# Performance work log

Hardware: AMD Instinct MI355X
Metric: run time of the kernel (lower is better)

The kernel has to match this reference:

```python
import jax, jax.numpy as jnp
import numpy as np

N_LAYERS = 2
N_COEF = 5
IN_DIM = 256
LN_EPS = 1e-6  # flax LayerNorm default


def jacobi_design(x, a, n):
    """Jacobi polynomials P_0..P_{n-1}^{(a,a)}(x). x: [...], returns [..., n]."""
    Ps = [jnp.ones_like(x)]
    if n > 1:
        Ps.append((a + 1.0) * x)
    for k in range(2, n):
        t = 2.0 * k + 2.0 * a
        A = 2.0 * k * (k + 2.0 * a) * (t - 2.0)
        B = (t - 1.0) * t * (t - 2.0)
        C = 2.0 * (k + a - 1.0) ** 2 * t
        Ps.append((B * x * Ps[-1] - C * Ps[-2]) / A)
    return jnp.stack(Ps, axis=-1)


def setup_inputs() -> dict:
    key = jax.random.key(0)
    k1, k2 = jax.random.split(key)
    x = jax.random.normal(k1, (8192, IN_DIM), dtype=jnp.float32)
    coefs = jax.random.normal(k2, (N_LAYERS, IN_DIM, IN_DIM, N_COEF), dtype=jnp.float32) * 0.03
    alphas = jnp.zeros((N_LAYERS,), dtype=jnp.float32)      # alpha_arctanh init zeros
    ln_scale = jnp.ones((N_LAYERS, IN_DIM), dtype=jnp.float32)
    ln_bias = jnp.zeros((N_LAYERS, IN_DIM), dtype=jnp.float32)
    return {"x": x, "coefs": coefs, "alphas": alphas, "ln_scale": ln_scale, "ln_bias": ln_bias}


def reference(x, coefs, alphas, ln_scale, ln_bias):
    h = x  # [B, D]
    for l in range(N_LAYERS):
        # LayerNorm
        mu = jnp.mean(h, axis=-1, keepdims=True)
        var = jnp.mean(jnp.square(h - mu), axis=-1, keepdims=True)
        hn = (h - mu) * jax.lax.rsqrt(var + LN_EPS) * ln_scale[l] + ln_bias[l]
        # KANLayer: Jacobi design matrix on tanh-mapped input
        a = jnp.tanh(alphas[l])
        dm = jacobi_design(jnp.tanh(hn), a, N_COEF)  # [B, D, C]
        # resid_scale=0, spline_scale=1, dropout inactive -> y = mean_i einsum
        in_dim = hn.shape[-1]
        h = jnp.einsum('bic,ioc->bo', dm, coefs[l]) / in_dim  # [B, D]
    return h
```

## Files before the change

kernel.cpp:

```cpp
#include <hip/hip_runtime.h>

#define D 256
#define NB 8192
#define NKC 128
#define PANEL (NKC * 512)

#define SXX_STRIDE 264
#define SXX_ELEMS (32 * SXX_STRIDE)
#define WREG 8192
#define SMEM_BYTES (SXX_ELEMS * 2 + 8 * WREG * 2)

typedef __bf16 bf16;
typedef bf16 bf16x8 __attribute__((ext_vector_type(8)));
typedef bf16 bf16x4 __attribute__((ext_vector_type(4)));
typedef float f32x4 __attribute__((ext_vector_type(4)));

__device__ __forceinline__ void glds16(const bf16* g, bf16* l) {
    __builtin_amdgcn_global_load_lds((const __attribute__((address_space(1))) void*)g,
                                     (__attribute__((address_space(3))) void*)l, 16, 0, 0);
}

__device__ __forceinline__ float fast_tanh(float x) {
    float e = __expf(2.f * x);
    return 1.f - 2.f / (e + 1.f);
}

__global__ __launch_bounds__(256) void pack_kernel(const float* __restrict__ coefs,
                                                   bf16* __restrict__ Wt,
                                                   float* __restrict__ beta) {
    __shared__ float t[64 * 65];
    __shared__ float accs[4][64];
    int b = blockIdx.x;
    if (b < 128) {
        int l = b >> 6, rem = b & 63;
        int c = (rem >> 4) + 1, tl = rem & 15;
        int plane = (c == 1) ? 0 : (c == 4) ? 1 : (c == 2) ? 2 : 3;
        int i0 = (tl >> 2) * 64, o0 = (tl & 3) * 64;

        for (int j = threadIdx.x; j < 4096; j += 256) {
            int i = j >> 6, o = j & 63;
            t[i * 65 + o] = coefs[(((size_t)(l * 256 + i0 + i)) * 256 + (o0 + o)) * 5 + c];
        }
        __syncthreads();
        bf16* dst = Wt + (size_t)l * (4 * PANEL)
                       + ((size_t)(tl & 3) * NKC + (plane * 256 + i0) / 8) * 512;
        for (int j = threadIdx.x; j < 4096; j += 256) {
            int il = j & 7, o = (j >> 3) & 63, ih = j >> 9;
            dst[j] = (bf16)t[(ih * 8 + il) * 65 + o];
        }
    } else {
        int lidx = b - 128;
        int l = lidx >> 2, o0 = (lidx & 3) * 64;
        int o = threadIdx.x & 63, ig = threadIdx.x >> 6;
        float sum = 0.f;
        for (int m = 0; m < 64; ++m) {
            int i = ig * 64 + m;
            sum += coefs[(((size_t)(l * 256 + i)) * 256 + (o0 + o)) * 5 + 0];
        }
        accs[ig][o] = sum;
        __syncthreads();
        if (threadIdx.x < 64)
            beta[l * 256 + o0 + threadIdx.x] = accs[0][threadIdx.x] + accs[1][threadIdx.x]
                                             + accs[2][threadIdx.x] + accs[3][threadIdx.x];
    }
}

template <int PH>
__device__ __forceinline__ void gemm_half(f32x4 (&acc)[2][4], const bf16* __restrict__ Wp,
                                          const bf16* sxx, bf16* sW, int l, float a1,
                                          float rB0, float rB1, float rB2,
                                          float rC0, float rC1, float rC2) {
    bf16x8 afn[2];
#pragma unroll
    for (int it = 0; it < 16; ++it) {
        if (it <= 13)      __builtin_amdgcn_s_waitcnt(0x0F78);
        else if (it == 14) __builtin_amdgcn_s_waitcnt(0x0F74);
        else               __builtin_amdgcn_s_waitcnt(0x0F70);
        const bf16* sWb = sW + (it & 3) * 2048;

        bf16x8 bfr[4];
#pragma unroll
        for (int tn = 0; tn < 4; ++tn)
            bfr[tn] = *(const bf16x8*)(sWb + (l >> 4) * 512 + (16 * tn + (l & 15)) * 8);

        bf16x8 af[2];
        if ((it & 1) == 0) {
            const int j  = it >> 1;
            const int i0 = j * 32 + (l >> 4) * 8;
#pragma unroll
            for (int tm = 0; tm < 2; ++tm) {
                bf16x8 xv = *(const bf16x8*)(sxx + (16 * tm + (l & 15)) * SXX_STRIDE + i0);
#pragma unroll
                for (int jj = 0; jj < 8; ++jj) {
                    float x  = (float)xv[jj];
                    float P1 = a1 * x;
                    float P2 = rB0 * x * P1 - rC0;
                    float P3 = rB1 * x * P2 - rC1 * P1;
                    float PA, PB;
                    if (PH == 0) { PA = P1; PB = rB2 * x * P3 - rC2 * P2; }
                    else         { PA = P2; PB = P3; }
                    af[tm][jj]  = (bf16)PA;
                    afn[tm][jj] = (bf16)PB;
                }
            }
        } else {
            af[0] = afn[0];
            af[1] = afn[1];
        }

#pragma unroll
        for (int tm = 0; tm < 2; ++tm)
#pragma unroll
            for (int tn = 0; tn < 4; ++tn)
                acc[tm][tn] = __builtin_amdgcn_mfma_f32_16x16x32_bf16(
                    af[tm], bfr[tn], acc[tm][tn], 0, 0, 0);

        if (it < 13) {
            __builtin_amdgcn_s_waitcnt(0xC47F);
            __builtin_amdgcn_sched_barrier(0);
            const int sidx  = it + 3;
            const int chunk = (PH * 2 + (sidx & 1)) * 8 + (sidx >> 1);
            bf16* dst = sW + (sidx & 3) * 2048;
#pragma unroll
            for (int t = 0; t < 4; ++t)
                glds16(Wp + chunk * 2048 + t * 512 + l * 8, dst + t * 512);
        }
    }
}

__global__ __launch_bounds__(512, 2) void fused2_kernel(
    const float* __restrict__ x, const float* __restrict__ ln_scale,
    const float* __restrict__ ln_bias, const float* __restrict__ alphas,
    const bf16* __restrict__ Wt, const float* __restrict__ beta,
    float* __restrict__ out) {
    extern __shared__ __align__(16) bf16 smem[];
    bf16* sxx  = smem;
    bf16* stag = smem + SXX_ELEMS;

    const int tid = threadIdx.x;
    const int l   = tid & 63;
    const int w   = tid >> 6;
    const int g   = w >> 1, p = w & 1;
    const int slab = blockIdx.x;

    bf16* sW = stag + w * WREG;

#pragma unroll
    for (int L = 0; L < 2; ++L) {
        const float* scale = ln_scale + L * D;
        const float* biasp = ln_bias + L * D;
        const bf16*  Wl    = Wt + (size_t)L * 4 * PANEL;
        const float* bet   = beta + L * D;

        const float a  = tanhf(alphas[L]);
        const float a1 = a + 1.f;
        float rB[3], rC[3];
#pragma unroll
        for (int k = 2; k < 5; k++) {
            float tk  = 2.f * k + 2.f * a;
            float iAk = 1.f / (2.f * k * (k + 2.f * a) * (tk - 2.f));
            rB[k - 2] = (tk - 1.f) * tk * (tk - 2.f) * iAk;
            rC[k - 2] = 2.f * (k + a - 1.f) * (k + a - 1.f) * tk * iAk;
        }

        float4 sc4 = ((const float4*)scale)[l];
        float4 bi4 = ((const float4*)biasp)[l];
        float scv[4] = {sc4.x, sc4.y, sc4.z, sc4.w};
        float biv[4] = {bi4.x, bi4.y, bi4.z, bi4.w};

#pragma unroll
        for (int rr = 0; rr < 4; ++rr) {
            int lr = w * 4 + rr;
            float4 v;
            if (L == 0) {
                v = ((const float4*)(x + ((size_t)slab * 32 + lr) * D))[l];
            } else {
                const float* hp = (const float*)(stag + (size_t)(l >> 4) * 2 * WREG);
                v = *(const float4*)(hp + lr * 64 + (l & 15) * 4);
            }
            float s  = v.x + v.y + v.z + v.w;
            float ss = v.x * v.x + v.y * v.y + v.z * v.z + v.w * v.w;
#pragma unroll
            for (int off = 32; off > 0; off >>= 1) {
                s  += __shfl_down(s, off);
                ss += __shfl_down(ss, off);
            }
            s  = __shfl(s, 0);
            ss = __shfl(ss, 0);
            float mu   = s * (1.f / D);
            float rstd = rsqrtf(ss * (1.f / D) - mu * mu + 1e-6f);
            float hv[4] = {v.x, v.y, v.z, v.w};
            bf16x4 o;
#pragma unroll
            for (int e = 0; e < 4; ++e)
                o[e] = (bf16)fast_tanh((hv[e] - mu) * rstd * scv[e] + biv[e]);
            *(bf16x4*)(sxx + lr * SXX_STRIDE + 4 * l) = o;
        }
        __syncthreads();

        const bf16* Wp = Wl + (size_t)g * PANEL;
#pragma unroll
        for (int s = 0; s < 3; ++s) {
            bf16* dst = sW + (s & 3) * 2048;
            const int chunk = (p * 2 + (s & 1)) * 8 + (s >> 1);
#pragma unroll
            for (int t = 0; t < 4; ++t)
                glds16(Wp + chunk * 2048 + t * 512 + l * 8, dst + t * 512);
        }

        f32x4 acc[2][4] = {};
        if (p == 0) gemm_half<0>(acc, Wp, sxx, sW, l, a1, rB[0], rB[1], rB[2], rC[0], rC[1], rC[2]);
        else        gemm_half<1>(acc, Wp, sxx, sW, l, a1, rB[0], rB[1], rB[2], rC[0], rC[1], rC[2]);

        if (p == 1) {
            f32x4* dumpr = (f32x4*)(stag + (size_t)w * WREG);
#pragma unroll
            for (int tm = 0; tm < 2; ++tm)
#pragma unroll
                for (int tn = 0; tn < 4; ++tn)
                    dumpr[(tm * 4 + tn) * 64 + l] = acc[tm][tn];
        }
        __syncthreads();

        if (p == 0) {
            f32x4* part = (f32x4*)(stag + (size_t)(w + 1) * WREG);
            if (L == 0) {
                float* hp = (float*)(stag + (size_t)w * WREG);
#pragma unroll
                for (int tm = 0; tm < 2; ++tm)
#pragma unroll
                    for (int tn = 0; tn < 4; ++tn) {
                        int lc = 16 * tn + (l & 15);
                        float bv = bet[g * 64 + lc] * (1.f / 256.f);
                        f32x4 v = acc[tm][tn] + part[(tm * 4 + tn) * 64 + l];
                        int lr0 = 16 * tm + (l >> 4) * 4;
#pragma unroll
                        for (int r = 0; r < 4; ++r)
                            hp[(lr0 + r) * 64 + lc] = v[r] * (1.f / 256.f) + bv;
                    }
            } else {
#pragma unroll
                for (int tm = 0; tm < 2; ++tm)
#pragma unroll
                    for (int tn = 0; tn < 4; ++tn) {
                        int gc = g * 64 + 16 * tn + (l & 15);
                        float bv = bet[gc] * (1.f / 256.f);
                        f32x4 v = acc[tm][tn] + part[(tm * 4 + tn) * 64 + l];
                        int gr = slab * 32 + 16 * tm + (l >> 4) * 4;
#pragma unroll
                        for (int r = 0; r < 4; ++r)
                            out[(size_t)(gr + r) * D + gc] = v[r] * (1.f / 256.f) + bv;
                    }
            }
        }
        __syncthreads();
    }
}

extern "C" void kernel_launch(void* const* d_in, const int* in_sizes, int n_in,
                              void* d_out, int out_size, void* d_ws, size_t ws_size,
                              hipStream_t stream) {
    const float* x        = (const float*)d_in[0];
    const float* coefs    = (const float*)d_in[1];
    const float* alphas   = (const float*)d_in[2];
    const float* ln_scale = (const float*)d_in[3];
    const float* ln_bias  = (const float*)d_in[4];
    float* out = (float*)d_out;

    char* ws = (char*)d_ws;
    bf16*  Wt   = (bf16*)ws;
    float* beta = (float*)(ws + 1048576);

    hipFuncSetAttribute((const void*)fused2_kernel,
                        hipFuncAttributeMaxDynamicSharedMemorySize, SMEM_BYTES);

    pack_kernel<<<136, 256, 0, stream>>>(coefs, Wt, beta);
    fused2_kernel<<<256, 512, SMEM_BYTES, stream>>>(x, ln_scale, ln_bias, alphas,
                                                    Wt, beta, out);
}
```

Before: 95.32 us.

## Load weight fragments directly from global into registers instead of LDS staging

Replaces the per-wave global_load_lds staging ring (with explicit waitcnt/sched_barrier) by direct global-to-register loads of B fragments into a 4-deep register ring, prefetched two iterations ahead. LDS per wave shrinks (WREG halved), and the LDS write/read round-trip and manual waitcnt are removed. In exchange it needs more VGPRs for the register ring, which may strain occupancy at 512x2 launch bounds, and leaves load latency hiding to the compiler.

```diff
diff --git a/kernel.cpp b/kernel.cpp
--- a/kernel.cpp
+++ b/kernel.cpp
@@ -7,18 +7,13 @@
 
 #define SXX_STRIDE 264
 #define SXX_ELEMS (32 * SXX_STRIDE)
-#define WREG 8192
+#define WREG 4096
 #define SMEM_BYTES (SXX_ELEMS * 2 + 8 * WREG * 2)
 
 typedef __bf16 bf16;
 typedef bf16 bf16x8 __attribute__((ext_vector_type(8)));
 typedef bf16 bf16x4 __attribute__((ext_vector_type(4)));
 typedef float f32x4 __attribute__((ext_vector_type(4)));
-
-__device__ __forceinline__ void glds16(const bf16* g, bf16* l) {
-    __builtin_amdgcn_global_load_lds((const __attribute__((address_space(1))) void*)g,
-                                     (__attribute__((address_space(3))) void*)l, 16, 0, 0);
-}
 
 __device__ __forceinline__ float fast_tanh(float x) {
     float e = __expf(2.f * x);
@@ -65,23 +60,23 @@
     }
 }
 
+#define CHOFF(PH, it) (((((PH) * 2 + ((it) & 1)) * 8) + ((it) >> 1)) * 2048)
+
 template <int PH>
-__device__ __forceinline__ void gemm_half(f32x4 (&acc)[2][4], const bf16* __restrict__ Wp,
-                                          const bf16* sxx, bf16* sW, int l, float a1,
+__device__ __forceinline__ void gemm_half(f32x4 (&acc)[2][4], bf16x8 (&wf)[4][4],
+                                          const bf16* __restrict__ lane,
+                                          const bf16* sxx, int l, float a1,
                                           float rB0, float rB1, float rB2,
                                           float rC0, float rC1, float rC2) {
     bf16x8 afn[2];
 #pragma unroll
     for (int it = 0; it < 16; ++it) {
-        if (it <= 13)      __builtin_amdgcn_s_waitcnt(0x0F78);
-        else if (it == 14) __builtin_amdgcn_s_waitcnt(0x0F74);
-        else               __builtin_amdgcn_s_waitcnt(0x0F70);
-        const bf16* sWb = sW + (it & 3) * 2048;
-
-        bf16x8 bfr[4];
-#pragma unroll
-        for (int tn = 0; tn < 4; ++tn)
-            bfr[tn] = *(const bf16x8*)(sWb + (l >> 4) * 512 + (16 * tn + (l & 15)) * 8);
+        if (it < 14) {
+            const int s = (it + 2) & 3;
+#pragma unroll
+            for (int tn = 0; tn < 4; ++tn)
+                wf[s][tn] = *(const bf16x8*)(lane + CHOFF(PH, it + 2) + tn * 128);
+        }
 
         bf16x8 af[2];
         if ((it & 1) == 0) {
@@ -108,23 +103,13 @@
             af[1] = afn[1];
         }
 
+        const int cur = it & 3;
 #pragma unroll
         for (int tm = 0; tm < 2; ++tm)
 #pragma unroll
             for (int tn = 0; tn < 4; ++tn)
                 acc[tm][tn] = __builtin_amdgcn_mfma_f32_16x16x32_bf16(
-                    af[tm], bfr[tn], acc[tm][tn], 0, 0, 0);
-
-        if (it < 13) {
-            __builtin_amdgcn_s_waitcnt(0xC47F);
-            __builtin_amdgcn_sched_barrier(0);
-            const int sidx  = it + 3;
-            const int chunk = (PH * 2 + (sidx & 1)) * 8 + (sidx >> 1);
-            bf16* dst = sW + (sidx & 3) * 2048;
-#pragma unroll
-            for (int t = 0; t < 4; ++t)
-                glds16(Wp + chunk * 2048 + t * 512 + l * 8, dst + t * 512);
-        }
+                    af[tm], wf[cur][tn], acc[tm][tn], 0, 0, 0);
     }
 }
 
@@ -143,14 +128,21 @@
     const int g   = w >> 1, p = w & 1;
     const int slab = blockIdx.x;
 
-    bf16* sW = stag + w * WREG;
-
 #pragma unroll
     for (int L = 0; L < 2; ++L) {
         const float* scale = ln_scale + L * D;
         const float* biasp = ln_bias + L * D;
         const bf16*  Wl    = Wt + (size_t)L * 4 * PANEL;
         const float* bet   = beta + L * D;
+
+        const bf16* lane = Wl + (size_t)g * PANEL + (l >> 4) * 512 + (l & 15) * 8;
+
+        bf16x8 wf[4][4];
+#pragma unroll
+        for (int s = 0; s < 2; ++s)
+#pragma unroll
+            for (int tn = 0; tn < 4; ++tn)
+                wf[s][tn] = *(const bf16x8*)(lane + (p * 16 + s * 8) * 2048 + tn * 128);
 
         const float a  = tanhf(alphas[L]);
         const float a1 = a + 1.f;
@@ -198,19 +190,9 @@
         }
         __syncthreads();
 
-        const bf16* Wp = Wl + (size_t)g * PANEL;
-#pragma unroll
-        for (int s = 0; s < 3; ++s) {
-            bf16* dst = sW + (s & 3) * 2048;
-            const int chunk = (p * 2 + (s & 1)) * 8 + (s >> 1);
-#pragma unroll
-            for (int t = 0; t < 4; ++t)
-                glds16(Wp + chunk * 2048 + t * 512 + l * 8, dst + t * 512);
-        }
-
         f32x4 acc[2][4] = {};
-        if (p == 0) gemm_half<0>(acc, Wp, sxx, sW, l, a1, rB[0], rB[1], rB[2], rC[0], rC[1], rC[2]);
-        else        gemm_half<1>(acc, Wp, sxx, sW, l, a1, rB[0], rB[1], rB[2], rC[0], rC[1], rC[2]);
+        if (p == 0) gemm_half<0>(acc, wf, lane, sxx, l, a1, rB[0], rB[1], rB[2], rC[0], rC[1], rC[2]);
+        else        gemm_half<1>(acc, wf, lane, sxx, l, a1, rB[0], rB[1], rB[2], rC[0], rC[1], rC[2]);
 
         if (p == 1) {
             f32x4* dumpr = (f32x4*)(stag + (size_t)w * WREG);
```

Result: no change. 93.79 us, median of 2 (-1.6%).
